# Performance work log

Hardware: AMD Instinct MI355X
Metric: run time of the kernel (lower is better)

Reference implementation:

```python
import jax, jax.numpy as jnp
import numpy as np

DIM = 2048
SEQ = 8192
NUM_HEADS = 16
PROJ_DIM = DIM // 4  # proj_ratio = 4.0
EPS = 1e-5


def setup_inputs() -> dict:
    key = jax.random.key(0)
    ks = jax.random.split(key, 8)
    s = 0.02  # param init scale
    return {
        "x": jax.random.normal(ks[0], (SEQ, DIM), jnp.float32),
        "q": jax.random.normal(ks[1], (1, DIM), jnp.float32),
        "W_kv": jax.random.normal(ks[2], (2 * DIM, DIM), jnp.float32) * s,
        "b_kv": jax.random.normal(ks[3], (2 * DIM,), jnp.float32) * s,
        "W_p1": jax.random.normal(ks[4], (PROJ_DIM, DIM), jnp.float32) * s,
        "b_p1": jax.random.normal(ks[5], (PROJ_DIM,), jnp.float32) * s,
        "W_p2": jax.random.normal(ks[6], (DIM, PROJ_DIM), jnp.float32) * s,
        "b_p2": jax.random.normal(ks[7], (DIM,), jnp.float32) * s,
        "ln_w": jnp.ones((PROJ_DIM,), jnp.float32),
        "ln_b": jnp.zeros((PROJ_DIM,), jnp.float32),
    }


def reference(x, q, W_kv, b_kv, W_p1, b_p1, W_p2, b_p2, ln_w, ln_b):
    seq, dim = x.shape
    h = NUM_HEADS
    d = dim // h

    # kv projection: [s, 2*dim]; split '(n h d)' with n leading -> k = first dim cols
    kv = x @ W_kv.T + b_kv
    k = kv[:, :dim].reshape(seq, h, d).transpose(1, 0, 2)   # [h, s, d]
    v = kv[:, dim:].reshape(seq, h, d).transpose(1, 0, 2)   # [h, s, d]
    qh = q.reshape(h, 1, d)                                  # '1 (h d) -> h 1 d'

    # single-query attention (qk_norm=False -> Identity norms)
    attn = jnp.einsum('hqd,hkd->hqk', qh, k) / jnp.sqrt(jnp.asarray(d, x.dtype))
    attn = jax.nn.softmax(attn, axis=-1)                     # [h, 1, s]
    x1 = jnp.einsum('hqk,hkd->hqd', attn, v)                 # [h, 1, d]
    x1 = x1.transpose(1, 0, 2).reshape(1, dim)               # 'h s d -> s (h d)'

    # proj MLP: proj1 -> LayerNorm -> relu -> proj2
    h1 = x1 @ W_p1.T + b_p1                                  # [1, proj_dim]
    mu = jnp.mean(h1, axis=-1, keepdims=True)
    var = jnp.mean(jnp.square(h1 - mu), axis=-1, keepdims=True)
    h1 = (h1 - mu) / jnp.sqrt(var + EPS) * ln_w + ln_b
    x1 = jax.nn.relu(h1) @ W_p2.T + b_p2                     # [1, dim]

    # residual broadcast: [s, dim] + [1, dim]
    return x + x1
```

## Files before the change

kernel.cpp:

```cpp
#include <hip/hip_runtime.h>
#include <math.h>

#define SEQ   8192
#define DIM   2048
#define NH    16
#define DH    128
#define PD    512

static constexpr float LN_EPS = 1e-5f;
static constexpr float SCALE  = 0.08838834764831845f;

typedef __bf16 bf16x8 __attribute__((ext_vector_type(8)));
typedef float  f32x4  __attribute__((ext_vector_type(4)));

static constexpr size_t OFF_QB   = 0;
static constexpr size_t OFF_SMP  = 16;
static constexpr size_t OFF_QWB  = 528;
static constexpr size_t OFF_ELOG = OFF_QWB + 16384;
static constexpr size_t OFF_PCTX = OFF_ELOG + 131072;
static constexpr size_t OFF_CTX  = OFF_PCTX + 128*32768;
static constexpr size_t OFF_X1   = OFF_CTX + 32768;
static constexpr size_t OFF_H1R  = OFF_X1 + 2048;
static constexpr size_t OFF_X1F  = OFF_H1R + 512;

__global__ __launch_bounds__(256) void k_prep(const float* __restrict__ q,
                                              const float* __restrict__ Wkv,
                                              const float* __restrict__ bkv,
                                              __bf16* __restrict__ qWb,
                                              float* __restrict__ qb,
                                              float* __restrict__ smp) {
    int t = threadIdx.x;
    int h = blockIdx.x >> 4, jc = blockIdx.x & 15;
    int col = t & 127, kh = t >> 7;
    int j = jc * 128 + col;
    const float* w  = Wkv + (size_t)(h * DH + kh * 64) * DIM + j;
    const float* qh = q + h * DH + kh * 64;
    float acc = 0.f;
#pragma unroll 16
    for (int d = 0; d < 64; ++d)
        acc += qh[d] * w[(size_t)d * DIM];
    __shared__ float part[128];
    if (kh) part[col] = acc;
    __syncthreads();
    if (!kh) qWb[h * DIM + j] = (__bf16)(acc + part[col]);
    if (jc == 0 && t < 64) {
        float p = q[h*DH + t] * bkv[h*DH + t] + q[h*DH + 64 + t] * bkv[h*DH + 64 + t];
        for (int off = 32; off; off >>= 1) p += __shfl_down(p, off);
        if (t == 0) qb[h] = p;
    }
    if (blockIdx.x == 0) { smp[t] = 0.f; smp[t + 256] = 0.f; }
}

__global__ __launch_bounds__(256) void k_logits(const float* __restrict__ x,
                                                const __bf16* __restrict__ qWb,
                                                const float* __restrict__ qb,
                                                float* __restrict__ elogT,
                                                float* __restrict__ smp) {
    const int t = threadIdx.x;
    const int w = t >> 6, lane = t & 63;
    const int r = lane & 15, quad = lane >> 4;
    const int s0 = blockIdx.x * 16;
    __shared__ float dpart[4][64][4];
    __shared__ float hsum[NH];
    if (t < NH) hsum[t] = 0.f;

    const float*  xrow = x + (size_t)(s0 + r) * DIM + quad * 8;
    const __bf16* brow = qWb + r * DIM + quad * 8;
    const int kbase = w * 512;

    f32x4 acc = {0.f, 0.f, 0.f, 0.f};
#pragma unroll 4
    for (int i = 0; i < 16; ++i) {
        int k = kbase + i * 32;
        float4 xa = *(const float4*)(xrow + k);
        float4 xb = *(const float4*)(xrow + k + 4);
        bf16x8 af;
        af[0] = (__bf16)xa.x; af[1] = (__bf16)xa.y;
        af[2] = (__bf16)xa.z; af[3] = (__bf16)xa.w;
        af[4] = (__bf16)xb.x; af[5] = (__bf16)xb.y;
        af[6] = (__bf16)xb.z; af[7] = (__bf16)xb.w;
        bf16x8 bf = *(const bf16x8*)(brow + k);
        acc = __builtin_amdgcn_mfma_f32_16x16x32_bf16(af, bf, acc, 0, 0, 0);
    }
    dpart[w][lane][0] = acc[0];
    dpart[w][lane][1] = acc[1];
    dpart[w][lane][2] = acc[2];
    dpart[w][lane][3] = acc[3];
    __syncthreads();

    {
        const int lane2 = t & 63, reg = t >> 6;
        const int h = lane2 & 15, sl = (lane2 >> 4) * 4 + reg;
        float v = dpart[0][lane2][reg] + dpart[1][lane2][reg]
                + dpart[2][lane2][reg] + dpart[3][lane2][reg];
        float e = __expf((v + qb[h]) * SCALE);
        elogT[(size_t)(s0 + sl) * NH + h] = e;
        atomicAdd(&hsum[h], e);
    }
    __syncthreads();
    if (t < NH) atomicAdd(&smp[t * 32 + (blockIdx.x & 31)], hsum[t]);
}

__global__ __launch_bounds__(256) void k_ctx(const float* __restrict__ x,
                                             const float* __restrict__ elogT,
                                             const float* __restrict__ smp,
                                             float* __restrict__ pctx) {
    int jc = blockIdx.x & 3, sc = blockIdx.x >> 2, t = threadIdx.x;
    int s0 = sc * 64;
    int j = jc * 512 + t * 2;
    __shared__ float inv_s[NH];
    __shared__ float att[64][NH];
    if (t < NH) {
        float S = 0.f;
#pragma unroll
        for (int i = 0; i < 32; ++i) S += smp[t * 32 + i];
        inv_s[t] = 1.0f / S;
    }
    __syncthreads();
    for (int i = t; i < 64 * NH; i += 256) {
        int rr = i >> 4, h = i & 15;
        att[rr][h] = elogT[(size_t)(s0 + rr) * NH + h] * inv_s[h];
    }
    __syncthreads();
    float2 acc[NH];
#pragma unroll
    for (int h = 0; h < NH; ++h) acc[h] = make_float2(0.f, 0.f);
    for (int rr = 0; rr < 64; ++rr) {
        float2 xv = *(const float2*)&x[(size_t)(s0 + rr) * DIM + j];
        const float4* ar = (const float4*)att[rr];
        float4 a0 = ar[0], a1 = ar[1], a2 = ar[2], a3 = ar[3];
        float aa[NH];
        *(float4*)&aa[0] = a0; *(float4*)&aa[4]  = a1;
        *(float4*)&aa[8] = a2; *(float4*)&aa[12] = a3;
#pragma unroll
        for (int h = 0; h < NH; ++h) {
            acc[h].x += aa[h] * xv.x;
            acc[h].y += aa[h] * xv.y;
        }
    }
#pragma unroll
    for (int h = 0; h < NH; ++h)
        *(float2*)&pctx[((size_t)(sc * NH + h)) * DIM + j] = acc[h];
}

__global__ __launch_bounds__(256) void k_ctxred(const float* __restrict__ pctx,
                                                float* __restrict__ ctx) {
    int idx = blockIdx.x * 256 + threadIdx.x;
    float s = 0.f;
#pragma unroll 8
    for (int sc = 0; sc < 128; ++sc)
        s += pctx[(size_t)sc * (NH * DIM) + idx];
    ctx[idx] = s;
}

__global__ __launch_bounds__(256) void k_x1(const float* __restrict__ Wkv,
                                            const float* __restrict__ bkv,
                                            const float* __restrict__ ctx,
                                            float* __restrict__ x1) {
    int row = blockIdx.x * 4 + (threadIdx.x >> 6);
    int lane = threadIdx.x & 63;
    const float* w = Wkv + (size_t)(DIM + row) * DIM;
    const float* c = ctx + (row >> 7) * DIM;
    float acc = 0.f;
#pragma unroll
    for (int k = 0; k < 8; ++k) {
        int j = k * 256 + lane * 4;
        float4 wv = *(const float4*)&w[j];
        float4 cv = *(const float4*)&c[j];
        acc += wv.x*cv.x + wv.y*cv.y + wv.z*cv.z + wv.w*cv.w;
    }
    for (int off = 32; off; off >>= 1) acc += __shfl_xor(acc, off);
    if (lane == 0) x1[row] = acc + bkv[DIM + row];
}

__global__ __launch_bounds__(256) void k_h1(const float* __restrict__ Wp1,
                                            const float* __restrict__ bp1,
                                            const float* __restrict__ x1,
                                            float* __restrict__ h1raw) {
    int row = blockIdx.x * 4 + (threadIdx.x >> 6);
    int lane = threadIdx.x & 63;
    const float* w = Wp1 + (size_t)row * DIM;
    float acc = 0.f;
#pragma unroll
    for (int k = 0; k < 8; ++k) {
        int j = k * 256 + lane * 4;
        float4 wv = *(const float4*)&w[j];
        float4 cv = *(const float4*)&x1[j];
        acc += wv.x*cv.x + wv.y*cv.y + wv.z*cv.z + wv.w*cv.w;
    }
    for (int off = 32; off; off >>= 1) acc += __shfl_xor(acc, off);
    if (lane == 0) h1raw[row] = acc + bp1[row];
}

__global__ __launch_bounds__(256) void k_x1f(const float* __restrict__ Wp2,
                                             const float* __restrict__ bp2,
                                             const float* __restrict__ h1raw,
                                             const float* __restrict__ lnw,
                                             const float* __restrict__ lnb,
                                             float* __restrict__ x1f) {
    int row = blockIdx.x * 4 + (threadIdx.x >> 6);
    int lane = threadIdx.x & 63;
    int j = lane * 8;
    float4 va = *(const float4*)&h1raw[j];
    float4 vb = *(const float4*)&h1raw[j + 4];
    float s = va.x + va.y + va.z + va.w + vb.x + vb.y + vb.z + vb.w;
    for (int off = 32; off; off >>= 1) s += __shfl_xor(s, off);
    float mu = s * (1.0f / PD);
    float dx[8];
    dx[0]=va.x-mu; dx[1]=va.y-mu; dx[2]=va.z-mu; dx[3]=va.w-mu;
    dx[4]=vb.x-mu; dx[5]=vb.y-mu; dx[6]=vb.z-mu; dx[7]=vb.w-mu;
    float s2 = 0.f;
#pragma unroll
    for (int i = 0; i < 8; ++i) s2 += dx[i] * dx[i];
    for (int off = 32; off; off >>= 1) s2 += __shfl_xor(s2, off);
    float rstd = rsqrtf(s2 * (1.0f / PD) + LN_EPS);
    float4 lw0 = *(const float4*)&lnw[j], lw1 = *(const float4*)&lnw[j + 4];
    float4 lb0 = *(const float4*)&lnb[j], lb1 = *(const float4*)&lnb[j + 4];
    float hln[8];
    hln[0]=fmaxf(dx[0]*rstd*lw0.x+lb0.x,0.f); hln[1]=fmaxf(dx[1]*rstd*lw0.y+lb0.y,0.f);
    hln[2]=fmaxf(dx[2]*rstd*lw0.z+lb0.z,0.f); hln[3]=fmaxf(dx[3]*rstd*lw0.w+lb0.w,0.f);
    hln[4]=fmaxf(dx[4]*rstd*lw1.x+lb1.x,0.f); hln[5]=fmaxf(dx[5]*rstd*lw1.y+lb1.y,0.f);
    hln[6]=fmaxf(dx[6]*rstd*lw1.z+lb1.z,0.f); hln[7]=fmaxf(dx[7]*rstd*lw1.w+lb1.w,0.f);
    const float* w = Wp2 + (size_t)row * PD + j;
    float4 w0 = *(const float4*)w, w1 = *(const float4*)(w + 4);
    float acc = w0.x*hln[0] + w0.y*hln[1] + w0.z*hln[2] + w0.w*hln[3]
              + w1.x*hln[4] + w1.y*hln[5] + w1.z*hln[6] + w1.w*hln[7];
    for (int off = 32; off; off >>= 1) acc += __shfl_xor(acc, off);
    if (lane == 0) x1f[row] = acc + bp2[row];
}

__global__ __launch_bounds__(256) void k_out(const float* __restrict__ x,
                                             const float* __restrict__ x1f,
                                             float* __restrict__ out) {
    size_t i = (size_t)blockIdx.x * 512 + threadIdx.x;
    float4 xv = ((const float4*)x)[i];
    float4 a  = ((const float4*)x1f)[(int)(i & 511)];
    ((float4*)out)[i] = make_float4(xv.x + a.x, xv.y + a.y, xv.z + a.z, xv.w + a.w);
    size_t i2 = i + 256;
    float4 xv2 = ((const float4*)x)[i2];
    float4 a2  = ((const float4*)x1f)[(int)(i2 & 511)];
    ((float4*)out)[i2] = make_float4(xv2.x + a2.x, xv2.y + a2.y, xv2.z + a2.z, xv2.w + a2.w);
}

extern "C" void kernel_launch(void* const* d_in, const int* in_sizes, int n_in,
                              void* d_out, int out_size, void* d_ws, size_t ws_size,
                              hipStream_t stream) {
    const float* x    = (const float*)d_in[0];
    const float* q    = (const float*)d_in[1];
    const float* Wkv  = (const float*)d_in[2];
    const float* bkv  = (const float*)d_in[3];
    const float* Wp1  = (const float*)d_in[4];
    const float* bp1  = (const float*)d_in[5];
    const float* Wp2  = (const float*)d_in[6];
    const float* bp2  = (const float*)d_in[7];
    const float* lnw  = (const float*)d_in[8];
    const float* lnb  = (const float*)d_in[9];
    float* out = (float*)d_out;
    float* ws  = (float*)d_ws;

    float*  qb    = ws + OFF_QB;
    float*  smp   = ws + OFF_SMP;
    __bf16* qWb   = (__bf16*)(ws + OFF_QWB);
    float*  elogT = ws + OFF_ELOG;
    float*  pctx  = ws + OFF_PCTX;
    float*  ctx   = ws + OFF_CTX;
    float*  x1    = ws + OFF_X1;
    float*  h1raw = ws + OFF_H1R;
    float*  x1f   = ws + OFF_X1F;

    k_prep  <<<256, 256, 0, stream>>>(q, Wkv, bkv, qWb, qb, smp);
    k_logits<<<512, 256, 0, stream>>>(x, qWb, qb, elogT, smp);
    k_ctx   <<<512, 256, 0, stream>>>(x, elogT, smp, pctx);
    k_ctxred<<<128, 256, 0, stream>>>(pctx, ctx);
    k_x1    <<<512, 256, 0, stream>>>(Wkv, bkv, ctx, x1);
    k_h1    <<<128, 256, 0, stream>>>(Wp1, bp1, x1, h1raw);
    k_x1f   <<<512, 256, 0, stream>>>(Wp2, bp2, h1raw, lnw, lnb, x1f);
    k_out   <<<8192, 256, 0, stream>>>(x, x1f, out);
}
```

Before: 222.2 us.

## Fuse logits and context accumulation into one attention kernel, defer normalization

Merges the logit/exp kernel and the context-accumulation kernel into one kernel that processes 32 rows per block. The exponentials stay in shared memory instead of a global buffer, and softmax normalization moves into the partial-context reduction. This removes one launch, the elogT round trip, and likely a second DRAM read of x. In exchange it doubles the partial-context buffer, halves the block count and raises register pressure with float4 accumulators for 16 heads.

```diff
diff --git a/kernel.cpp b/kernel.cpp
--- a/kernel.cpp
+++ b/kernel.cpp
@@ -16,9 +16,8 @@
 static constexpr size_t OFF_QB   = 0;
 static constexpr size_t OFF_SMP  = 16;
 static constexpr size_t OFF_QWB  = 528;
-static constexpr size_t OFF_ELOG = OFF_QWB + 16384;
-static constexpr size_t OFF_PCTX = OFF_ELOG + 131072;
-static constexpr size_t OFF_CTX  = OFF_PCTX + 128*32768;
+static constexpr size_t OFF_PCTX = OFF_QWB + 16384;
+static constexpr size_t OFF_CTX  = OFF_PCTX + 256*32768;
 static constexpr size_t OFF_X1   = OFF_CTX + 32768;
 static constexpr size_t OFF_H1R  = OFF_X1 + 2048;
 static constexpr size_t OFF_X1F  = OFF_H1R + 512;
@@ -51,106 +50,106 @@
     if (blockIdx.x == 0) { smp[t] = 0.f; smp[t + 256] = 0.f; }
 }
 
-__global__ __launch_bounds__(256) void k_logits(const float* __restrict__ x,
-                                                const __bf16* __restrict__ qWb,
-                                                const float* __restrict__ qb,
-                                                float* __restrict__ elogT,
-                                                float* __restrict__ smp) {
+__global__ __launch_bounds__(256) void k_attn(const float* __restrict__ x,
+                                              const __bf16* __restrict__ qWb,
+                                              const float* __restrict__ qb,
+                                              float* __restrict__ pctx,
+                                              float* __restrict__ smp) {
     const int t = threadIdx.x;
     const int w = t >> 6, lane = t & 63;
     const int r = lane & 15, quad = lane >> 4;
-    const int s0 = blockIdx.x * 16;
+    const int s0 = blockIdx.x * 32;
+    const int tile = w >> 1, kh = w & 1;
     __shared__ float dpart[4][64][4];
+    __shared__ float att[32][NH];
     __shared__ float hsum[NH];
     if (t < NH) hsum[t] = 0.f;
 
-    const float*  xrow = x + (size_t)(s0 + r) * DIM + quad * 8;
+    const float*  xrow = x + (size_t)(s0 + tile * 16 + r) * DIM + quad * 8;
     const __bf16* brow = qWb + r * DIM + quad * 8;
-    const int kbase = w * 512;
-
-    f32x4 acc = {0.f, 0.f, 0.f, 0.f};
+    const int kbase = kh * 1024;
+    f32x4 acc0 = {0.f, 0.f, 0.f, 0.f}, acc1 = {0.f, 0.f, 0.f, 0.f};
 #pragma unroll 4
     for (int i = 0; i < 16; ++i) {
-        int k = kbase + i * 32;
-        float4 xa = *(const float4*)(xrow + k);
-        float4 xb = *(const float4*)(xrow + k + 4);
-        bf16x8 af;
-        af[0] = (__bf16)xa.x; af[1] = (__bf16)xa.y;
-        af[2] = (__bf16)xa.z; af[3] = (__bf16)xa.w;
-        af[4] = (__bf16)xb.x; af[5] = (__bf16)xb.y;
-        af[6] = (__bf16)xb.z; af[7] = (__bf16)xb.w;
-        bf16x8 bf = *(const bf16x8*)(brow + k);
-        acc = __builtin_amdgcn_mfma_f32_16x16x32_bf16(af, bf, acc, 0, 0, 0);
-    }
-    dpart[w][lane][0] = acc[0];
-    dpart[w][lane][1] = acc[1];
-    dpart[w][lane][2] = acc[2];
-    dpart[w][lane][3] = acc[3];
+        int k = kbase + i * 64;
+        {
+            float4 xa = *(const float4*)(xrow + k);
+            float4 xb = *(const float4*)(xrow + k + 4);
+            bf16x8 af;
+            af[0]=(__bf16)xa.x; af[1]=(__bf16)xa.y; af[2]=(__bf16)xa.z; af[3]=(__bf16)xa.w;
+            af[4]=(__bf16)xb.x; af[5]=(__bf16)xb.y; af[6]=(__bf16)xb.z; af[7]=(__bf16)xb.w;
+            bf16x8 bfv = *(const bf16x8*)(brow + k);
+            acc0 = __builtin_amdgcn_mfma_f32_16x16x32_bf16(af, bfv, acc0, 0, 0, 0);
+        }
+        {
+            float4 xa = *(const float4*)(xrow + k + 32);
+            float4 xb = *(const float4*)(xrow + k + 36);
+            bf16x8 af;
+            af[0]=(__bf16)xa.x; af[1]=(__bf16)xa.y; af[2]=(__bf16)xa.z; af[3]=(__bf16)xa.w;
+            af[4]=(__bf16)xb.x; af[5]=(__bf16)xb.y; af[6]=(__bf16)xb.z; af[7]=(__bf16)xb.w;
+            bf16x8 bfv = *(const bf16x8*)(brow + k + 32);
+            acc1 = __builtin_amdgcn_mfma_f32_16x16x32_bf16(af, bfv, acc1, 0, 0, 0);
+        }
+    }
+    dpart[w][lane][0] = acc0[0] + acc1[0];
+    dpart[w][lane][1] = acc0[1] + acc1[1];
+    dpart[w][lane][2] = acc0[2] + acc1[2];
+    dpart[w][lane][3] = acc0[3] + acc1[3];
     __syncthreads();
-
     {
         const int lane2 = t & 63, reg = t >> 6;
         const int h = lane2 & 15, sl = (lane2 >> 4) * 4 + reg;
-        float v = dpart[0][lane2][reg] + dpart[1][lane2][reg]
-                + dpart[2][lane2][reg] + dpart[3][lane2][reg];
-        float e = __expf((v + qb[h]) * SCALE);
-        elogT[(size_t)(s0 + sl) * NH + h] = e;
-        atomicAdd(&hsum[h], e);
+        float v0 = dpart[0][lane2][reg] + dpart[1][lane2][reg];
+        float e0 = __expf((v0 + qb[h]) * SCALE);
+        att[sl][h] = e0;
+        float v1 = dpart[2][lane2][reg] + dpart[3][lane2][reg];
+        float e1 = __expf((v1 + qb[h]) * SCALE);
+        att[16 + sl][h] = e1;
+        atomicAdd(&hsum[h], e0 + e1);
     }
     __syncthreads();
     if (t < NH) atomicAdd(&smp[t * 32 + (blockIdx.x & 31)], hsum[t]);
-}
-
-__global__ __launch_bounds__(256) void k_ctx(const float* __restrict__ x,
-                                             const float* __restrict__ elogT,
-                                             const float* __restrict__ smp,
-                                             float* __restrict__ pctx) {
-    int jc = blockIdx.x & 3, sc = blockIdx.x >> 2, t = threadIdx.x;
-    int s0 = sc * 64;
-    int j = jc * 512 + t * 2;
-    __shared__ float inv_s[NH];
-    __shared__ float att[64][NH];
-    if (t < NH) {
-        float S = 0.f;
-#pragma unroll
-        for (int i = 0; i < 32; ++i) S += smp[t * 32 + i];
-        inv_s[t] = 1.0f / S;
-    }
-    __syncthreads();
-    for (int i = t; i < 64 * NH; i += 256) {
-        int rr = i >> 4, h = i & 15;
-        att[rr][h] = elogT[(size_t)(s0 + rr) * NH + h] * inv_s[h];
-    }
-    __syncthreads();
-    float2 acc[NH];
-#pragma unroll
-    for (int h = 0; h < NH; ++h) acc[h] = make_float2(0.f, 0.f);
-    for (int rr = 0; rr < 64; ++rr) {
-        float2 xv = *(const float2*)&x[(size_t)(s0 + rr) * DIM + j];
-        const float4* ar = (const float4*)att[rr];
-        float4 a0 = ar[0], a1 = ar[1], a2 = ar[2], a3 = ar[3];
-        float aa[NH];
-        *(float4*)&aa[0] = a0; *(float4*)&aa[4]  = a1;
-        *(float4*)&aa[8] = a2; *(float4*)&aa[12] = a3;
-#pragma unroll
-        for (int h = 0; h < NH; ++h) {
-            acc[h].x += aa[h] * xv.x;
-            acc[h].y += aa[h] * xv.y;
+
+#pragma unroll
+    for (int jc = 0; jc < 2; ++jc) {
+        int j = jc * 1024 + t * 4;
+        float4 acc[NH];
+#pragma unroll
+        for (int h = 0; h < NH; ++h) acc[h] = make_float4(0.f, 0.f, 0.f, 0.f);
+        for (int rr = 0; rr < 32; ++rr) {
+            float4 xv = *(const float4*)&x[(size_t)(s0 + rr) * DIM + j];
+            const float4* ar = (const float4*)att[rr];
+            float4 a0 = ar[0], a1 = ar[1], a2 = ar[2], a3 = ar[3];
+            float aa[NH];
+            *(float4*)&aa[0] = a0; *(float4*)&aa[4]  = a1;
+            *(float4*)&aa[8] = a2; *(float4*)&aa[12] = a3;
+#pragma unroll
+            for (int h = 0; h < NH; ++h) {
+                acc[h].x += aa[h] * xv.x;
+                acc[h].y += aa[h] * xv.y;
+                acc[h].z += aa[h] * xv.z;
+                acc[h].w += aa[h] * xv.w;
+            }
         }
-    }
-#pragma unroll
-    for (int h = 0; h < NH; ++h)
-        *(float2*)&pctx[((size_t)(sc * NH + h)) * DIM + j] = acc[h];
+#pragma unroll
+        for (int h = 0; h < NH; ++h)
+            *(float4*)&pctx[((size_t)(blockIdx.x * NH + h)) * DIM + j] = acc[h];
+    }
 }
 
 __global__ __launch_bounds__(256) void k_ctxred(const float* __restrict__ pctx,
+                                                const float* __restrict__ smp,
                                                 float* __restrict__ ctx) {
     int idx = blockIdx.x * 256 + threadIdx.x;
+    int h = idx >> 11;
+    float S = 0.f;
+#pragma unroll
+    for (int i = 0; i < 32; ++i) S += smp[h * 32 + i];
     float s = 0.f;
 #pragma unroll 8
-    for (int sc = 0; sc < 128; ++sc)
+    for (int sc = 0; sc < 256; ++sc)
         s += pctx[(size_t)sc * (NH * DIM) + idx];
-    ctx[idx] = s;
+    ctx[idx] = s / S;
 }
 
 __global__ __launch_bounds__(256) void k_x1(const float* __restrict__ Wkv,
@@ -261,7 +260,6 @@
     float*  qb    = ws + OFF_QB;
     float*  smp   = ws + OFF_SMP;
     __bf16* qWb   = (__bf16*)(ws + OFF_QWB);
-    float*  elogT = ws + OFF_ELOG;
     float*  pctx  = ws + OFF_PCTX;
     float*  ctx   = ws + OFF_CTX;
     float*  x1    = ws + OFF_X1;
@@ -269,9 +267,8 @@
     float*  x1f   = ws + OFF_X1F;
 
     k_prep  <<<256, 256, 0, stream>>>(q, Wkv, bkv, qWb, qb, smp);
-    k_logits<<<512, 256, 0, stream>>>(x, qWb, qb, elogT, smp);
-    k_ctx   <<<512, 256, 0, stream>>>(x, elogT, smp, pctx);
-    k_ctxred<<<128, 256, 0, stream>>>(pctx, ctx);
+    k_attn  <<<256, 256, 0, stream>>>(x, qWb, qb, pctx, smp);
+    k_ctxred<<<128, 256, 0, stream>>>(pctx, smp, ctx);
     k_x1    <<<512, 256, 0, stream>>>(Wkv, bkv, ctx, x1);
     k_h1    <<<128, 256, 0, stream>>>(Wp1, bp1, x1, h1raw);
     k_x1f   <<<512, 256, 0, stream>>>(Wp2, bp2, h1raw, lnw, lnb, x1f);
```

Result: no change. 225.1 us (+1.3%).
